# Performance work log

Hardware: AMD Instinct MI355X
Metric: run time of the kernel (lower is better)

Reference implementation:

```python
import jax, jax.numpy as jnp
import numpy as np

C = 1024      # n_feature // 2
OUT = 128     # out_dim
B, T, F = 16, 512, 2048


def conv1d(x, w, b):
    # x: [B, C, T], w: [O, I, 3], padding=1 stride=1 (torch Conv1d semantics)
    y = jax.lax.conv_general_dilated(x, w, window_strides=(1,), padding=[(1, 1)],
                                     dimension_numbers=('NCH', 'OIH', 'NCH'))
    return y + b[None, :, None]


def setup_inputs() -> dict:
    key = jax.random.key(0)
    ks = jax.random.split(key, 20)
    s = 0.02
    inp = {
        'inputs': jax.random.normal(ks[0], (B, T, F), jnp.float32),
        'wq': jax.random.normal(ks[1], (C, C, 3), jnp.float32) * s,
        'bq': jnp.zeros((C,), jnp.float32),
        'wk': jax.random.normal(ks[2], (C, C, 3), jnp.float32) * s,
        'bk': jnp.zeros((C,), jnp.float32),
        'wv': jax.random.normal(ks[3], (C, C, 3), jnp.float32) * s,
        'bv': jnp.zeros((C,), jnp.float32),
        'gamma': jax.random.normal(ks[4], (), jnp.float32) * 0.5,
        'w_fcf': jax.random.normal(ks[5], (C, C), jnp.float32) * s,
        'b_fcf': jnp.zeros((C,), jnp.float32),
        'w_fc1f': jax.random.normal(ks[6], (OUT, C), jnp.float32) * s,
        'b_fc1f': jnp.zeros((OUT,), jnp.float32),
        'w_fcr': jax.random.normal(ks[7], (C, C), jnp.float32) * s,
        'b_fcr': jnp.zeros((C,), jnp.float32),
        'w_fc1r': jax.random.normal(ks[8], (OUT, C), jnp.float32) * s,
        'b_fc1r': jnp.zeros((OUT,), jnp.float32),
        'inputs_len': jax.random.randint(ks[9], (B,), 64, T, dtype=jnp.int32),
        'is_query': 1,
    }
    return inp


def reference(inputs, wq, bq, wk, bk, wv, bv, gamma,
              w_fcf, b_fcf, w_fc1f, b_fc1f, w_fcr, b_fcr, w_fc1r, b_fc1r,
              inputs_len, is_query):
    nby2 = inputs.shape[-1] // 2
    base_x_f = inputs[:, :, nby2:]
    base_x_r = inputs[:, :, :nby2]

    def ragged_self_att(x):
        # x: [B, T, C]; attention only over each sample's first q_len frames,
        # remaining frames passed through untouched (matches per-sample slicing).
        b, t, c = x.shape
        pos = jnp.arange(t)
        mask = pos[None, :] < inputs_len[:, None]            # [B, T]
        xm = x * mask[..., None]                              # zero beyond q_len => conv zero-pad semantics at boundary
        xc = jnp.transpose(xm, (0, 2, 1))                     # [B, C, T]
        q = jnp.transpose(conv1d(xc, wq, bq), (0, 2, 1))      # [B, T, C]
        k = conv1d(xc, wk, bk)                                # [B, C, T]
        v = conv1d(xc, wv, bv)                                # [B, C, T]
        scale = jnp.sqrt(inputs_len.astype(x.dtype))[:, None, None]  # sqrt(dep)=sqrt(q_len)
        scores = jnp.einsum('btc,bcs->bts', q, k) / scale     # [B, T, T]
        scores = jnp.where(mask[:, None, :], scores, -jnp.inf)
        attn = jax.nn.softmax(scores, axis=-1)
        out = jnp.einsum('bcs,bts->btc', v, attn)             # bmm(v, attn^T), transposed to [B,T,C]
        feat = gamma * out + xm
        return jnp.where(mask[..., None], feat, x)

    a_f = ragged_self_att(base_x_f)
    a_r = ragged_self_att(base_x_r)

    def head(x, w1, b1, w2, b2):
        h = jax.nn.relu(jnp.einsum('btc,oc->bto', x, w1) + b1)
        # dropout skipped (eval / deterministic reference)
        return jax.nn.relu(jnp.einsum('btc,oc->bto', h, w2) + b2)

    y_f = head(a_f, w_fcf, b_fcf, w_fc1f, b_fc1f)
    y_r = head(a_r, w_fcr, b_fcr, w_fc1r, b_fc1r)
    return jnp.concatenate([y_f, y_r], axis=-1)              # [B, T, 2*OUT]
```

## Files before the change

### kernel.cpp

```cpp
#include <hip/hip_runtime.h>
#include <hip/hip_bf16.h>

typedef unsigned short u16;
typedef __attribute__((ext_vector_type(8))) __bf16 bf16x8;
typedef __attribute__((ext_vector_type(4))) float f32x4;

__device__ __forceinline__ u16 f2b(float f) {
  __hip_bfloat16 h = __float2bfloat16(f);
  u16 u;
  __builtin_memcpy(&u, &h, 2);
  return u;
}

__device__ __forceinline__ void gload16(const void* g, void* l) {
  __builtin_amdgcn_global_load_lds(
      (const __attribute__((address_space(1))) unsigned int*)g,
      (__attribute__((address_space(3))) unsigned int*)l, 16, 0, 0);
}

enum { OP_CONV = 0, OP_SCORES = 2, OP_PV = 3, OP_HEAD1 = 4, OP_HEAD2 = 5 };

struct GP {
  const u16* A;
  const u16* Bt;
  int lda, ldb, K, mbase;
  long sAz, sBz;
  void* out;
  void* out2;
  void* out3;
  const float* bias;
  const float* bias2;
  const float* bias3;
  const float* gamma;
  const float* x_full;
  const int* lens;
  const u16* zpage;
};

template <int TAG>
__global__ __launch_bounds__(256, 4) void gemm_k(GP p) {
  __shared__ __align__(16) u16 As[128 * 64];
  __shared__ __align__(16) u16 Bs[128 * 64];

  const int tid = threadIdx.x;
  const int lane = tid & 63;
  const int w = tid >> 6;
  const int wr = (w >> 1) * 64;
  const int wc = (w & 1) * 64;
  const int m0 = blockIdx.y * 128;
  const int n0 = blockIdx.x * 128;
  const int z = blockIdx.z;

  const u16* Ab = p.A + (long)z * p.sAz;
  const u16* Bb = p.Bt + (long)z * p.sBz;

  const int sr = tid >> 3;
  const int scs = (((tid & 7) ^ ((tid >> 3) & 7)) << 3);

  f32x4 acc[4][4] = {};

  for (int k0 = 0; k0 < p.K; k0 += 64) {
#pragma unroll
    for (int R = 0; R < 4; ++R) {
      const int row = R * 32 + sr;
      const u16* srcA;
      if constexpr (TAG == OP_CONV) {
        const int hrow = m0 + row;
        const int b = hrow >> 9;
        const int t = (hrow & 511) + (k0 >> 10) - 1;
        const int ii = (k0 & 1023) + scs;
        srcA = ((unsigned)t < 512u) ? (Ab + (((long)(b << 9) + t) << 10) + ii)
                                    : (p.zpage + scs);
      } else {
        srcA = Ab + (long)(m0 + row) * p.lda + (k0 + scs);
      }
      gload16(srcA, (char*)As + R * 4096 + w * 1024);
      const u16* srcB = Bb + (long)(n0 + row) * p.ldb + (k0 + scs);
      gload16(srcB, (char*)Bs + R * 4096 + w * 1024);
    }
    __syncthreads();
#pragma unroll
    for (int kk = 0; kk < 64; kk += 32) {
      const int kc = kk + (lane >> 4) * 8;
      const int slot = kc >> 3;
      bf16x8 aF[4], bF[4];
#pragma unroll
      for (int mi = 0; mi < 4; ++mi) {
        const int r = wr + mi * 16 + (lane & 15);
        aF[mi] = *(const bf16x8*)(As + r * 64 + ((slot ^ (r & 7)) << 3));
      }
#pragma unroll
      for (int ni = 0; ni < 4; ++ni) {
        const int r = wc + ni * 16 + (lane & 15);
        bF[ni] = *(const bf16x8*)(Bs + r * 64 + ((slot ^ (r & 7)) << 3));
      }
#pragma unroll
      for (int mi = 0; mi < 4; ++mi)
#pragma unroll
        for (int ni = 0; ni < 4; ++ni)
          acc[mi][ni] = __builtin_amdgcn_mfma_f32_16x16x32_bf16(
              aF[mi], bF[ni], acc[mi][ni], 0, 0, 0);
    }
    __syncthreads();
  }

  const int fr = (lane >> 4) * 4;
  const int fc = lane & 15;

  if constexpr (TAG == OP_CONV) {
    const int opid = n0 >> 10;
    const int nc = n0 & 1023;
    const float* bp = (opid == 0) ? p.bias : (opid == 1) ? p.bias2 : p.bias3;
#pragma unroll
    for (int ni = 0; ni < 4; ++ni) {
      const int col = nc + wc + ni * 16 + fc;
      const float bsv = bp[col];
#pragma unroll
      for (int mi = 0; mi < 4; ++mi)
#pragma unroll
        for (int j = 0; j < 4; ++j) {
          const int grow = p.mbase + m0 + wr + mi * 16 + fr + j;
          const u16 v = f2b(acc[mi][ni][j] + bsv);
          if (opid == 0) ((u16*)p.out)[(long)grow * 1024 + col] = v;
          else if (opid == 1) ((u16*)p.out2)[(long)grow * 1024 + col] = v;
          else ((u16*)p.out3)[((long)(grow >> 9) * 1024 + col) * 512 + (grow & 511)] = v;
        }
    }
  } else if constexpr (TAG == OP_SCORES) {
    float* op = (float*)p.out + (long)z * 262144;
#pragma unroll
    for (int ni = 0; ni < 4; ++ni) {
      const int col = n0 + wc + ni * 16 + fc;
#pragma unroll
      for (int mi = 0; mi < 4; ++mi)
#pragma unroll
        for (int j = 0; j < 4; ++j) {
          const int row = m0 + wr + mi * 16 + fr + j;
          op[(long)row * 512 + col] = acc[mi][ni][j];
        }
    }
  } else if constexpr (TAG == OP_PV) {
    u16* op = (u16*)p.out;
    const int half = z >> 4, b = z & 15;
    const int len = p.lens[b];
    const float g = *p.gamma;
    const float* xb = p.x_full + ((long)b * 512) * 2048 + (half == 0 ? 1024 : 0);
#pragma unroll
    for (int ni = 0; ni < 4; ++ni) {
      const int col = n0 + wc + ni * 16 + fc;
#pragma unroll
      for (int mi = 0; mi < 4; ++mi)
#pragma unroll
        for (int j = 0; j < 4; ++j) {
          const int t = m0 + wr + mi * 16 + fr + j;
          const float xv = xb[(long)t * 2048 + col];
          const float r = (t < len) ? fmaf(g, acc[mi][ni][j], xv) : xv;
          op[((long)z * 512 + t) * 1024 + col] = f2b(r);
        }
    }
  } else if constexpr (TAG == OP_HEAD1) {
    u16* op = (u16*)p.out;
    const float* bp = (z == 0) ? p.bias : p.bias2;
#pragma unroll
    for (int ni = 0; ni < 4; ++ni) {
      const int col = n0 + wc + ni * 16 + fc;
      const float bsv = bp[col];
#pragma unroll
      for (int mi = 0; mi < 4; ++mi)
#pragma unroll
        for (int j = 0; j < 4; ++j) {
          const int row = m0 + wr + mi * 16 + fr + j;
          op[((long)z * 8192 + row) * 1024 + col] = f2b(fmaxf(acc[mi][ni][j] + bsv, 0.f));
        }
    }
  } else {
    float* op = (float*)p.out;
    const float* bp = (z == 0) ? p.bias : p.bias2;
#pragma unroll
    for (int ni = 0; ni < 4; ++ni) {
      const int col = wc + ni * 16 + fc;
      const float bsv = bp[col];
#pragma unroll
      for (int mi = 0; mi < 4; ++mi)
#pragma unroll
        for (int j = 0; j < 4; ++j) {
          const int row = m0 + wr + mi * 16 + fr + j;
          op[(long)row * 256 + z * 128 + col] = fmaxf(acc[mi][ni][j] + bsv, 0.f);
        }
    }
  }
}

__global__ __launch_bounds__(256) void softmax_k(const float* scores, u16* attn,
                                                 const int* lens) {
  const int row = blockIdx.x * 4 + (threadIdx.x >> 6);
  const int lane = threadIdx.x & 63;
  const int len = lens[row >> 9];
  const float inv = rsqrtf((float)len);
  const float* sr = scores + (long)row * 512;
  u16* ar = attn + (long)row * 512;
  float e[8];
  float mx = -1e30f;
#pragma unroll
  for (int j = 0; j < 8; ++j) {
    const int s = j * 64 + lane;
    const float v = (s < len) ? sr[s] * inv : -1e30f;
    e[j] = v;
    mx = fmaxf(mx, v);
  }
#pragma unroll
  for (int d = 1; d < 64; d <<= 1) mx = fmaxf(mx, __shfl_xor(mx, d));
  float sum = 0.f;
#pragma unroll
  for (int j = 0; j < 8; ++j) {
    const int s = j * 64 + lane;
    const float t = (s < len) ? __expf(e[j] - mx) : 0.f;
    e[j] = t;
    sum += t;
  }
#pragma unroll
  for (int d = 1; d < 64; d <<= 1) sum += __shfl_xor(sum, d);
  const float r = 1.f / sum;
#pragma unroll
  for (int j = 0; j < 8; ++j) ar[j * 64 + lane] = f2b(e[j] * r);
}

__global__ void convw_k(const float* wsrc, u16* wt) {
  const int idx = blockIdx.x * 256 + threadIdx.x;
  const float* s = wsrc + (long)idx * 3;
  u16* d = wt + (long)(idx >> 10) * 3072 + (idx & 1023);
  d[0] = f2b(s[0]);
  d[1024] = f2b(s[1]);
  d[2048] = f2b(s[2]);
}

__global__ void castk(const float* s, u16* d, int n) {
  const int i = blockIdx.x * 256 + threadIdx.x;
  if (i < n) d[i] = f2b(s[i]);
}

__global__ void xmk(const float* inputs, u16* xm, const int* lens, int xoff) {
  const int idx = blockIdx.x * 256 + threadIdx.x;
  const int row = idx >> 8;
  const int c4 = (idx & 255) * 4;
  const bool live = (row & 511) < lens[row >> 9];
  float4 v = {0.f, 0.f, 0.f, 0.f};
  if (live) v = *(const float4*)(inputs + (long)row * 2048 + xoff + c4);
  ushort4 o;
  o.x = f2b(v.x); o.y = f2b(v.y); o.z = f2b(v.z); o.w = f2b(v.w);
  *(ushort4*)(xm + (long)row * 1024 + c4) = o;
}

__global__ void zerok(u16* p) { p[blockIdx.x * 256 + threadIdx.x] = 0; }

extern "C" void kernel_launch(void* const* d_in, const int* in_sizes, int n_in,
                              void* d_out, int out_size, void* d_ws, size_t ws_size,
                              hipStream_t stream) {
  const float* inputs = (const float*)d_in[0];
  const float* wq = (const float*)d_in[1];
  const float* bq = (const float*)d_in[2];
  const float* wk = (const float*)d_in[3];
  const float* bk = (const float*)d_in[4];
  const float* wv = (const float*)d_in[5];
  const float* bv = (const float*)d_in[6];
  const float* gamma = (const float*)d_in[7];
  const float* w_fcf = (const float*)d_in[8];
  const float* b_fcf = (const float*)d_in[9];
  const float* w_fc1f = (const float*)d_in[10];
  const float* b_fc1f = (const float*)d_in[11];
  const float* w_fcr = (const float*)d_in[12];
  const float* b_fcr = (const float*)d_in[13];
  const float* w_fc1r = (const float*)d_in[14];
  const float* b_fc1r = (const float*)d_in[15];
  const int* lens = (const int*)d_in[16];
  float* out = (float*)d_out;

  char* ws = (char*)d_ws;
  size_t off = 0;
  auto alloc = [&](size_t n) {
    char* p = ws + off;
    off += (n + 255) & ~(size_t)255;
    return p;
  };

  u16* wt_all = (u16*)alloc(3072l * 3072 * 2);
  u16* w1b = (u16*)alloc(2l * 1024 * 1024 * 2);
  u16* w2b = (u16*)alloc(2l * 128 * 1024 * 2);
  u16* zpage = (u16*)alloc(4096);
  u16* xm = (u16*)alloc(8192l * 1024 * 2);
  u16* qb = (u16*)alloc(16384l * 1024 * 2);
  u16* kb = (u16*)alloc(16384l * 1024 * 2);
  u16* vb = (u16*)alloc(32l * 1024 * 512 * 2);
  u16* attn = wt_all;
  float* scores = (float*)xm;
  u16* abuf = qb;
  u16* hbuf = kb;

  zerok<<<8, 256, 0, stream>>>(zpage);
  convw_k<<<4096, 256, 0, stream>>>(wq, wt_all);
  convw_k<<<4096, 256, 0, stream>>>(wk, wt_all + 1024l * 3072);
  convw_k<<<4096, 256, 0, stream>>>(wv, wt_all + 2048l * 3072);
  castk<<<4096, 256, 0, stream>>>(w_fcf, w1b, 1024 * 1024);
  castk<<<4096, 256, 0, stream>>>(w_fcr, w1b + 1024l * 1024, 1024 * 1024);
  castk<<<512, 256, 0, stream>>>(w_fc1f, w2b, 128 * 1024);
  castk<<<512, 256, 0, stream>>>(w_fc1r, w2b + 128l * 1024, 128 * 1024);

  for (int half = 0; half < 2; ++half) {
    const int xoff = (half == 0) ? 1024 : 0;
    xmk<<<8192, 256, 0, stream>>>(inputs, xm, lens, xoff);
    GP g{};
    g.zpage = zpage;
    g.A = xm; g.Bt = wt_all; g.lda = 1024; g.ldb = 3072; g.K = 3072;
    g.mbase = half * 8192; g.sAz = 0; g.sBz = 0;
    g.out = qb; g.out2 = kb; g.out3 = vb;
    g.bias = bq; g.bias2 = bk; g.bias3 = bv;
    gemm_k<OP_CONV><<<dim3(24, 64, 1), 256, 0, stream>>>(g);
  }

  for (int half = 0; half < 2; ++half) {
    GP g{};
    g.A = qb + (long)half * 8192 * 1024;
    g.Bt = kb + (long)half * 8192 * 1024;
    g.lda = 1024; g.ldb = 1024; g.K = 1024;
    g.sAz = 512l * 1024; g.sBz = 512l * 1024;
    g.out = scores;
    gemm_k<OP_SCORES><<<dim3(4, 4, 16), 256, 0, stream>>>(g);
    softmax_k<<<2048, 256, 0, stream>>>(scores, attn + (long)half * 8192 * 512, lens);
  }

  {
    GP g{};
    g.A = attn; g.Bt = vb; g.lda = 512; g.ldb = 512; g.K = 512;
    g.sAz = 512l * 512; g.sBz = 1024l * 512;
    g.out = abuf; g.gamma = gamma; g.x_full = inputs; g.lens = lens;
    gemm_k<OP_PV><<<dim3(8, 4, 32), 256, 0, stream>>>(g);
  }

  {
    GP g{};
    g.A = abuf; g.Bt = w1b; g.lda = 1024; g.ldb = 1024; g.K = 1024;
    g.sAz = 8192l * 1024; g.sBz = 1024l * 1024;
    g.out = hbuf; g.bias = b_fcf; g.bias2 = b_fcr;
    gemm_k<OP_HEAD1><<<dim3(8, 64, 2), 256, 0, stream>>>(g);
  }

  {
    GP g{};
    g.A = hbuf; g.Bt = w2b; g.lda = 1024; g.ldb = 1024; g.K = 1024;
    g.sAz = 8192l * 1024; g.sBz = 128l * 1024;
    g.out = out; g.bias = b_fc1f; g.bias2 = b_fc1r;
    gemm_k<OP_HEAD2><<<dim3(1, 64, 2), 256, 0, stream>>>(g);
  }
}
```

Before: 705.6 us.

## Add 256x256 double-buffered GEMM kernel for conv and head1, merge halves

Introduces a new 512-thread GEMM kernel with 256x256 tiles, a 128KB double-buffered LDS pipeline that prefetches the next K-tile while issuing MFMAs, setprio around the compute phases, and an XCD-aware block remapping. It replaces the 128x128 kernel for the fused QKV conv GEMM and the first head GEMM. The two input halves are also merged into single launches for masking, conv, scores and softmax, with workspace buffers reshuffled to fit. The aim is higher MFMA utilization and fewer launches, at the cost of higher LDS and register use per block, which limits occupancy.

```diff
diff --git a/kernel.cpp b/kernel.cpp
--- a/kernel.cpp
+++ b/kernel.cpp
@@ -18,23 +18,178 @@
       (__attribute__((address_space(3))) unsigned int*)l, 16, 0, 0);
 }
 
-enum { OP_CONV = 0, OP_SCORES = 2, OP_PV = 3, OP_HEAD1 = 4, OP_HEAD2 = 5 };
-
-struct GP {
+__device__ __forceinline__ bf16x8 ldsA(const char* base, int row, int ch) {
+  return *(const bf16x8*)(base + row * 128 + ((ch ^ (row & 7)) << 4));
+}
+
+struct G2 {
   const u16* A;
   const u16* Bt;
-  int lda, ldb, K, mbase;
-  long sAz, sBz;
+  const u16* Bt2;
   void* out;
   void* out2;
   void* out3;
   const float* bias;
   const float* bias2;
   const float* bias3;
+  const u16* zpage;
+  int K;
+};
+
+#define STAGE_A(kt, bi)                                                        \
+  {                                                                            \
+    _Pragma("unroll") for (int r_ = 0; r_ < 4; ++r_) {                         \
+      const int idx_ = r_ * 512 + tid;                                         \
+      const int row_ = idx_ >> 3;                                              \
+      const int k_ = (kt) * 64 + (((idx_ & 7) ^ (row_ & 7)) << 3);             \
+      const u16* src_;                                                         \
+      if constexpr (TAG == 0) {                                                \
+        const int gm_ = m0 + row_;                                             \
+        const int t_ = (gm_ & 511) + (k_ >> 10) - 1;                           \
+        src_ = ((unsigned)t_ < 512u)                                           \
+                   ? p.A + ((((long)(gm_ >> 9) << 9) + t_) << 10) + (k_ & 1023)\
+                   : p.zpage;                                                  \
+      } else {                                                                 \
+        src_ = p.A + (long)(m0 + row_) * 1024 + k_;                            \
+      }                                                                        \
+      gload16(src_, (char*)lds + (bi) * 65536 + r_ * 8192 + w * 1024);         \
+    }                                                                          \
+  }
+
+#define STAGE_B(kt, bi)                                                        \
+  {                                                                            \
+    _Pragma("unroll") for (int r_ = 0; r_ < 4; ++r_) {                         \
+      const int idx_ = r_ * 512 + tid;                                         \
+      const int row_ = idx_ >> 3;                                              \
+      const int k_ = (kt) * 64 + (((idx_ & 7) ^ (row_ & 7)) << 3);             \
+      const u16* src_ = Bb + (long)(n0 + row_) * LDB + k_;                     \
+      gload16(src_, (char*)lds + (bi) * 65536 + 32768 + r_ * 8192 + w * 1024); \
+    }                                                                          \
+  }
+
+#define PHASE(bi, qm, s, LOADB, STAGE_CODE)                                    \
+  {                                                                            \
+    const char* Ab_ = (const char*)lds + (bi) * 65536;                         \
+    bf16x8 aF[4];                                                              \
+    const int ch_ = (s) * 4 + (lane >> 4);                                     \
+    const int r0_ = wr * 128 + (qm) * 64 + (lane & 15);                        \
+    _Pragma("unroll") for (int fi = 0; fi < 4; ++fi)                           \
+        aF[fi] = ldsA(Ab_, r0_ + fi * 16, ch_);                                \
+    if (LOADB) {                                                               \
+      const int rb_ = wc * 64 + (lane & 15);                                   \
+      _Pragma("unroll") for (int ni = 0; ni < 4; ++ni)                         \
+          bF[ni] = ldsA(Ab_ + 32768, rb_ + ni * 16, ch_);                      \
+    }                                                                          \
+    STAGE_CODE                                                                 \
+    __builtin_amdgcn_s_barrier();                                              \
+    __builtin_amdgcn_s_setprio(1);                                             \
+    _Pragma("unroll") for (int fi = 0; fi < 4; ++fi)                           \
+        _Pragma("unroll") for (int ni = 0; ni < 4; ++ni)                       \
+            acc[(qm) * 4 + fi][ni] = __builtin_amdgcn_mfma_f32_16x16x32_bf16(  \
+                aF[fi], bF[ni], acc[(qm) * 4 + fi][ni], 0, 0, 0);              \
+    __builtin_amdgcn_s_setprio(0);                                             \
+  }
+
+template <int TAG>
+__global__ __launch_bounds__(512, 2) void gemm256_k(G2 p) {
+  __shared__ __align__(16) char lds[2 * 65536];
+
+  constexpr int NTN = (TAG == 0) ? 12 : 4;
+  constexpr int LDB = (TAG == 0) ? 3072 : 1024;
+
+  const int tid = threadIdx.x;
+  const int lane = tid & 63;
+  const int w = tid >> 6;
+  const int wr = w >> 2;
+  const int wc = w & 3;
+
+  const int cpx = gridDim.x >> 3;
+  const int wg = (blockIdx.x & 7) * cpx + (blockIdx.x >> 3);
+  const int n0 = (wg % NTN) * 256;
+  const int m0 = (wg / NTN) * 256;
+
+  const u16* Bb = (TAG == 1 && m0 >= 8192) ? p.Bt2 : p.Bt;
+
+  const int NT = p.K >> 6;
+
+  f32x4 acc[8][4] = {};
+  bf16x8 bF[4];
+
+  STAGE_A(0, 0);
+  STAGE_B(0, 0);
+  asm volatile("s_waitcnt vmcnt(0)" ::: "memory");
+  __builtin_amdgcn_s_barrier();
+
+  for (int t = 0; t < NT; ++t) {
+    const int bi = t & 1;
+    const bool pf = (t + 1 < NT);
+    PHASE(bi, 0, 0, true, { if (pf) STAGE_A(t + 1, bi ^ 1); });
+    __builtin_amdgcn_s_barrier();
+    PHASE(bi, 1, 0, false, { if (pf) STAGE_B(t + 1, bi ^ 1); });
+    __builtin_amdgcn_s_barrier();
+    PHASE(bi, 0, 1, true, {});
+    __builtin_amdgcn_s_barrier();
+    PHASE(bi, 1, 1, false, {});
+    asm volatile("s_waitcnt vmcnt(0)" ::: "memory");
+    __builtin_amdgcn_s_barrier();
+  }
+
+  const int fr = (lane >> 4) * 4;
+  const int fc = lane & 15;
+
+  if constexpr (TAG == 0) {
+    const int opid = n0 >> 10;
+    const int nc = n0 & 1023;
+    const float* bp = (opid == 0) ? p.bias : (opid == 1) ? p.bias2 : p.bias3;
+    u16* qo = (u16*)p.out;
+    u16* ko = (u16*)p.out2;
+    u16* vo = (u16*)p.out3;
+#pragma unroll
+    for (int ni = 0; ni < 4; ++ni) {
+      const int col = nc + wc * 64 + ni * 16 + fc;
+      const float bsv = bp[col];
+#pragma unroll
+      for (int mi = 0; mi < 8; ++mi)
+#pragma unroll
+        for (int j = 0; j < 4; ++j) {
+          const int grow = m0 + wr * 128 + mi * 16 + fr + j;
+          const u16 v = f2b(acc[mi][ni][j] + bsv);
+          if (opid == 0) qo[(long)grow * 1024 + col] = v;
+          else if (opid == 1) ko[(long)grow * 1024 + col] = v;
+          else vo[((long)(grow >> 9) * 1024 + col) * 512 + (grow & 511)] = v;
+        }
+    }
+  } else {
+    const float* bp = (m0 >> 13) ? p.bias2 : p.bias;
+    u16* ho = (u16*)p.out;
+#pragma unroll
+    for (int ni = 0; ni < 4; ++ni) {
+      const int col = n0 + wc * 64 + ni * 16 + fc;
+      const float bsv = bp[col];
+#pragma unroll
+      for (int mi = 0; mi < 8; ++mi)
+#pragma unroll
+        for (int j = 0; j < 4; ++j) {
+          const int grow = m0 + wr * 128 + mi * 16 + fr + j;
+          ho[(long)grow * 1024 + col] = f2b(fmaxf(acc[mi][ni][j] + bsv, 0.f));
+        }
+    }
+  }
+}
+
+enum { OP_SCORES = 2, OP_PV = 3, OP_HEAD2 = 5 };
+
+struct GP {
+  const u16* A;
+  const u16* Bt;
+  int lda, ldb, K;
+  long sAz, sBz;
+  void* out;
+  const float* bias;
+  const float* bias2;
   const float* gamma;
   const float* x_full;
   const int* lens;
-  const u16* zpage;
 };
 
 template <int TAG>
@@ -63,17 +218,7 @@
 #pragma unroll
     for (int R = 0; R < 4; ++R) {
       const int row = R * 32 + sr;
-      const u16* srcA;
-      if constexpr (TAG == OP_CONV) {
-        const int hrow = m0 + row;
-        const int b = hrow >> 9;
-        const int t = (hrow & 511) + (k0 >> 10) - 1;
-        const int ii = (k0 & 1023) + scs;
-        srcA = ((unsigned)t < 512u) ? (Ab + (((long)(b << 9) + t) << 10) + ii)
-                                    : (p.zpage + scs);
-      } else {
-        srcA = Ab + (long)(m0 + row) * p.lda + (k0 + scs);
-      }
+      const u16* srcA = Ab + (long)(m0 + row) * p.lda + (k0 + scs);
       gload16(srcA, (char*)As + R * 4096 + w * 1024);
       const u16* srcB = Bb + (long)(n0 + row) * p.ldb + (k0 + scs);
       gload16(srcB, (char*)Bs + R * 4096 + w * 1024);
@@ -81,8 +226,7 @@
     __syncthreads();
 #pragma unroll
     for (int kk = 0; kk < 64; kk += 32) {
-      const int kc = kk + (lane >> 4) * 8;
-      const int slot = kc >> 3;
+      const int slot = (kk >> 3) + (lane >> 4);
       bf16x8 aF[4], bF[4];
 #pragma unroll
       for (int mi = 0; mi < 4; ++mi) {
@@ -107,26 +251,7 @@
   const int fr = (lane >> 4) * 4;
   const int fc = lane & 15;
 
-  if constexpr (TAG == OP_CONV) {
-    const int opid = n0 >> 10;
-    const int nc = n0 & 1023;
-    const float* bp = (opid == 0) ? p.bias : (opid == 1) ? p.bias2 : p.bias3;
-#pragma unroll
-    for (int ni = 0; ni < 4; ++ni) {
-      const int col = nc + wc + ni * 16 + fc;
-      const float bsv = bp[col];
-#pragma unroll
-      for (int mi = 0; mi < 4; ++mi)
-#pragma unroll
-        for (int j = 0; j < 4; ++j) {
-          const int grow = p.mbase + m0 + wr + mi * 16 + fr + j;
-          const u16 v = f2b(acc[mi][ni][j] + bsv);
-          if (opid == 0) ((u16*)p.out)[(long)grow * 1024 + col] = v;
-          else if (opid == 1) ((u16*)p.out2)[(long)grow * 1024 + col] = v;
-          else ((u16*)p.out3)[((long)(grow >> 9) * 1024 + col) * 512 + (grow & 511)] = v;
-        }
-    }
-  } else if constexpr (TAG == OP_SCORES) {
+  if constexpr (TAG == OP_SCORES) {
     float* op = (float*)p.out + (long)z * 262144;
 #pragma unroll
     for (int ni = 0; ni < 4; ++ni) {
@@ -158,21 +283,6 @@
           op[((long)z * 512 + t) * 1024 + col] = f2b(r);
         }
     }
-  } else if constexpr (TAG == OP_HEAD1) {
-    u16* op = (u16*)p.out;
-    const float* bp = (z == 0) ? p.bias : p.bias2;
-#pragma unroll
-    for (int ni = 0; ni < 4; ++ni) {
-      const int col = n0 + wc + ni * 16 + fc;
-      const float bsv = bp[col];
-#pragma unroll
-      for (int mi = 0; mi < 4; ++mi)
-#pragma unroll
-        for (int j = 0; j < 4; ++j) {
-          const int row = m0 + wr + mi * 16 + fr + j;
-          op[((long)z * 8192 + row) * 1024 + col] = f2b(fmaxf(acc[mi][ni][j] + bsv, 0.f));
-        }
-    }
   } else {
     float* op = (float*)p.out;
     const float* bp = (z == 0) ? p.bias : p.bias2;
@@ -195,7 +305,7 @@
                                                  const int* lens) {
   const int row = blockIdx.x * 4 + (threadIdx.x >> 6);
   const int lane = threadIdx.x & 63;
-  const int len = lens[row >> 9];
+  const int len = lens[(row >> 9) & 15];
   const float inv = rsqrtf((float)len);
   const float* sr = scores + (long)row * 512;
   u16* ar = attn + (long)row * 512;
@@ -239,13 +349,14 @@
   if (i < n) d[i] = f2b(s[i]);
 }
 
-__global__ void xmk(const float* inputs, u16* xm, const int* lens, int xoff) {
+__global__ void xmk(const float* inputs, u16* xm, const int* lens) {
   const int idx = blockIdx.x * 256 + threadIdx.x;
   const int row = idx >> 8;
   const int c4 = (idx & 255) * 4;
-  const bool live = (row & 511) < lens[row >> 9];
+  const int xoff = (row & 8192) ? 0 : 1024;
+  const bool live = (row & 511) < lens[(row >> 9) & 15];
   float4 v = {0.f, 0.f, 0.f, 0.f};
-  if (live) v = *(const float4*)(inputs + (long)row * 2048 + xoff + c4);
+  if (live) v = *(const float4*)(inputs + (long)(row & 8191) * 2048 + xoff + c4);
   ushort4 o;
   o.x = f2b(v.x); o.y = f2b(v.y); o.z = f2b(v.z); o.w = f2b(v.w);
   *(ushort4*)(xm + (long)row * 1024 + c4) = o;
@@ -284,15 +395,15 @@
   };
 
   u16* wt_all = (u16*)alloc(3072l * 3072 * 2);
-  u16* w1b = (u16*)alloc(2l * 1024 * 1024 * 2);
-  u16* w2b = (u16*)alloc(2l * 128 * 1024 * 2);
   u16* zpage = (u16*)alloc(4096);
-  u16* xm = (u16*)alloc(8192l * 1024 * 2);
+  u16* xm = (u16*)alloc(16384l * 1024 * 2);
   u16* qb = (u16*)alloc(16384l * 1024 * 2);
   u16* kb = (u16*)alloc(16384l * 1024 * 2);
   u16* vb = (u16*)alloc(32l * 1024 * 512 * 2);
   u16* attn = wt_all;
   float* scores = (float*)xm;
+  u16* w1b = (u16*)xm;
+  u16* w2b = w1b + 2l * 1024 * 1024;
   u16* abuf = qb;
   u16* hbuf = kb;
 
@@ -300,33 +411,28 @@
   convw_k<<<4096, 256, 0, stream>>>(wq, wt_all);
   convw_k<<<4096, 256, 0, stream>>>(wk, wt_all + 1024l * 3072);
   convw_k<<<4096, 256, 0, stream>>>(wv, wt_all + 2048l * 3072);
+  xmk<<<16384, 256, 0, stream>>>(inputs, xm, lens);
+
+  {
+    G2 g{};
+    g.A = xm; g.Bt = wt_all; g.zpage = zpage; g.K = 3072;
+    g.out = qb; g.out2 = kb; g.out3 = vb;
+    g.bias = bq; g.bias2 = bk; g.bias3 = bv;
+    gemm256_k<0><<<768, 512, 0, stream>>>(g);
+  }
+
+  {
+    GP g{};
+    g.A = qb; g.Bt = kb; g.lda = 1024; g.ldb = 1024; g.K = 1024;
+    g.sAz = 512l * 1024; g.sBz = 512l * 1024; g.out = scores;
+    gemm_k<OP_SCORES><<<dim3(4, 4, 32), 256, 0, stream>>>(g);
+  }
+  softmax_k<<<4096, 256, 0, stream>>>(scores, attn, lens);
+
   castk<<<4096, 256, 0, stream>>>(w_fcf, w1b, 1024 * 1024);
   castk<<<4096, 256, 0, stream>>>(w_fcr, w1b + 1024l * 1024, 1024 * 1024);
   castk<<<512, 256, 0, stream>>>(w_fc1f, w2b, 128 * 1024);
   castk<<<512, 256, 0, stream>>>(w_fc1r, w2b + 128l * 1024, 128 * 1024);
-
-  for (int half = 0; half < 2; ++half) {
-    const int xoff = (half == 0) ? 1024 : 0;
-    xmk<<<8192, 256, 0, stream>>>(inputs, xm, lens, xoff);
-    GP g{};
-    g.zpage = zpage;
-    g.A = xm; g.Bt = wt_all; g.lda = 1024; g.ldb = 3072; g.K = 3072;
-    g.mbase = half * 8192; g.sAz = 0; g.sBz = 0;
-    g.out = qb; g.out2 = kb; g.out3 = vb;
-    g.bias = bq; g.bias2 = bk; g.bias3 = bv;
-    gemm_k<OP_CONV><<<dim3(24, 64, 1), 256, 0, stream>>>(g);
-  }
-
-  for (int half = 0; half < 2; ++half) {
-    GP g{};
-    g.A = qb + (long)half * 8192 * 1024;
-    g.Bt = kb + (long)half * 8192 * 1024;
-    g.lda = 1024; g.ldb = 1024; g.K = 1024;
-    g.sAz = 512l * 1024; g.sBz = 512l * 1024;
-    g.out = scores;
-    gemm_k<OP_SCORES><<<dim3(4, 4, 16), 256, 0, stream>>>(g);
-    softmax_k<<<2048, 256, 0, stream>>>(scores, attn + (long)half * 8192 * 512, lens);
-  }
 
   {
     GP g{};
@@ -337,11 +443,10 @@
   }
 
   {
-    GP g{};
-    g.A = abuf; g.Bt = w1b; g.lda = 1024; g.ldb = 1024; g.K = 1024;
-    g.sAz = 8192l * 1024; g.sBz = 1024l * 1024;
-    g.out = hbuf; g.bias = b_fcf; g.bias2 = b_fcr;
-    gemm_k<OP_HEAD1><<<dim3(8, 64, 2), 256, 0, stream>>>(g);
+    G2 h{};
+    h.A = abuf; h.Bt = w1b; h.Bt2 = w1b + 1024l * 1024; h.K = 1024;
+    h.out = hbuf; h.bias = b_fcf; h.bias2 = b_fcr;
+    gemm256_k<1><<<256, 512, 0, stream>>>(h);
   }
 
   {
```

After: 694.7 us. No clear change (-1.5%).
